# Performance work log

Measured on AMD Instinct MI355X. Metric: run time of the kernel, lower is better.

Reference implementation:

```python
import jax, jax.numpy as jnp
import numpy as np
import math

B, S, D, G, H_SEQ = 8, 4096, 1024, 64, 2048
TOP_K = 8


def setup_inputs() -> dict:
    key = jax.random.key(0)
    ks = jax.random.split(key, 10)
    K_curr = jax.random.normal(ks[0], (B, S, D), dtype=jnp.float32)
    V_curr = jax.random.normal(ks[1], (B, S, D), dtype=jnp.float32)
    K_prev = jax.random.normal(ks[2], (B, S, D), dtype=jnp.float32)
    V_prev = jax.random.normal(ks[3], (B, S, D), dtype=jnp.float32)
    h = jax.random.normal(ks[4], (B, H_SEQ, D), dtype=jnp.float32)
    momentum = jax.random.uniform(ks[5], (B, 1), dtype=jnp.float32)
    # unique active indices per batch (torch.scatter with dup idx is undefined)
    idx_keys = jax.random.split(ks[6], B)
    active_idx = jax.vmap(lambda k: jax.random.permutation(k, S)[:G])(idx_keys).astype(jnp.int32)
    # gate projection params: Linear(2, G), bias init = log(top_k - 1)
    Wk = jax.random.normal(ks[7], (G, 2), dtype=jnp.float32) * (1.0 / math.sqrt(2.0))
    Wv = jax.random.normal(ks[8], (G, 2), dtype=jnp.float32) * (1.0 / math.sqrt(2.0))
    bias_val = math.log(max(TOP_K - 1, 1))
    bk = jnp.full((G,), bias_val, dtype=jnp.float32)
    bv = jnp.full((G,), bias_val, dtype=jnp.float32)
    eta_init = 1.0 - 1.0 / H_SEQ
    logit_eta = jnp.asarray(math.log(eta_init / (1.0 - eta_init)), dtype=jnp.float32)
    alpha_logit = jnp.zeros((1,), dtype=jnp.float32)
    return {
        "K_curr": K_curr, "V_curr": V_curr, "K_prev": K_prev, "V_prev": V_prev,
        "h": h, "momentum": momentum, "active_idx": active_idx,
        "Wk": Wk, "bk": bk, "Wv": Wv, "bv": bv,
        "logit_eta": logit_eta, "alpha_logit": alpha_logit,
    }


def reference(K_curr, V_curr, K_prev, V_prev, h, momentum, active_idx,
              Wk, bk, Wv, bv, logit_eta, alpha_logit):
    scale = D ** (-0.5)
    idx = active_idx[..., None]  # [B, G, 1]
    # gather active slots: [B, G, D]
    K_active = jnp.take_along_axis(K_curr, idx, axis=1)
    K_prev_a = jnp.take_along_axis(K_prev, idx, axis=1)
    V_active = jnp.take_along_axis(V_curr, idx, axis=1)
    V_prev_a = jnp.take_along_axis(V_prev, idx, axis=1)

    q_probe = jnp.mean(h, axis=1)  # [B, D]

    def probe_surprise(X):
        # single-query attention probe over G slots
        attn = jax.nn.softmax(jnp.einsum('bd,bgd->bg', q_probe, X) * scale, axis=-1)
        pred = jnp.einsum('bg,bgd->bd', attn, X)
        return jnp.mean((pred - q_probe) ** 2, axis=-1, keepdims=True)  # [B, 1]

    k_surprise = probe_surprise(K_active)
    v_surprise = probe_surprise(V_active)

    alpha = jax.nn.sigmoid(alpha_logit)  # [1]
    combined = alpha * k_surprise + (1.0 - alpha) * v_surprise
    eta = jax.nn.sigmoid(logit_eta)
    new_momentum = eta * momentum + (1.0 - eta) * combined  # [B, 1]

    k_in = jnp.concatenate([k_surprise, new_momentum], axis=-1)  # [B, 2]
    v_in = jnp.concatenate([v_surprise, new_momentum], axis=-1)
    k_gate = jax.nn.sigmoid(k_in @ Wk.T + bk)[..., None]  # [B, G, 1]
    v_gate = jax.nn.sigmoid(v_in @ Wv.T + bv)[..., None]

    K_gated_a = k_gate * K_active + (1.0 - k_gate) * K_prev_a
    V_gated_a = v_gate * V_active + (1.0 - v_gate) * V_prev_a

    b_idx = jnp.arange(B)[:, None]  # [B, 1]
    K_gated = K_curr.at[b_idx, active_idx].set(K_gated_a)
    V_gated = V_curr.at[b_idx, active_idx].set(V_gated_a)
    return K_gated, V_gated, new_momentum
```

## Files before the change

kernel.cpp:

```cpp
#include <hip/hip_runtime.h>

#define BB 8
#define SS 4096
#define DD 1024
#define D4 256
#define GG 64
#define HH 2048
#define NCH 64
#define SCALE 0.03125f
#define BSD (8L * 4096L * 1024L)

__device__ __forceinline__ float sigmoidf_(float x) {
    return 1.0f / (1.0f + expf(-x));
}

__global__ __launch_bounds__(256) void reduce_h(const float* __restrict__ h,
                                                float* __restrict__ partial) {
    int blk = blockIdx.x;
    int b  = blk >> 6;
    int ch = blk & 63;
    int t  = threadIdx.x;
    const float4* h4 = (const float4*)h;
    int sbase = ch * (HH / NCH);
    long base = ((long)b * HH + sbase) * D4 + t;
    float4 acc = make_float4(0.f, 0.f, 0.f, 0.f);
#pragma unroll 4
    for (int i = 0; i < HH / NCH; ++i) {
        float4 v = h4[base + (long)i * D4];
        acc.x += v.x; acc.y += v.y; acc.z += v.z; acc.w += v.w;
    }
    ((float4*)partial)[(long)blk * D4 + t] = acc;
}

__global__ __launch_bounds__(256) void probe_kernel(
        const float* __restrict__ K_curr, const float* __restrict__ V_curr,
        const float* __restrict__ momentum, const int* __restrict__ active_idx,
        const float* __restrict__ Wk, const float* __restrict__ bk,
        const float* __restrict__ Wv, const float* __restrict__ bv,
        const float* __restrict__ logit_eta, const float* __restrict__ alpha_logit,
        const float* __restrict__ partial,
        float* __restrict__ gate_k, float* __restrict__ gate_v,
        float* __restrict__ out_m) {
    int b = blockIdx.x;
    int t = threadIdx.x;
    int wave = t >> 6;
    int lane = t & 63;

    __shared__ float q[DD];
    __shared__ float lg[GG];
    __shared__ float attn[GG];
    __shared__ float red[4];
    __shared__ float s_sur[2];

    float4 acc = make_float4(0.f, 0.f, 0.f, 0.f);
    const float4* p4 = (const float4*)partial;
#pragma unroll 8
    for (int ch = 0; ch < NCH; ++ch) {
        float4 v = p4[(long)(b * NCH + ch) * D4 + t];
        acc.x += v.x; acc.y += v.y; acc.z += v.z; acc.w += v.w;
    }
    const float invH = 1.0f / (float)HH;
    acc.x *= invH; acc.y *= invH; acc.z *= invH; acc.w *= invH;
    ((float4*)q)[t] = acc;
    __syncthreads();

    for (int which = 0; which < 2; ++which) {
        const float* X = which ? V_curr : K_curr;

        for (int gi = 0; gi < 16; ++gi) {
            int g = wave * 16 + gi;
            int idx = active_idx[b * GG + g];
            const float* row = X + ((long)b * SS + idx) * DD;
            float s = 0.f;
#pragma unroll
            for (int j = 0; j < 16; ++j) {
                int d = lane + 64 * j;
                s += q[d] * row[d];
            }
#pragma unroll
            for (int off = 32; off >= 1; off >>= 1) s += __shfl_xor(s, off);
            if (lane == 0) lg[g] = s * SCALE;
        }
        __syncthreads();

        if (t < 64) {
            float x = lg[t];
            float m = x;
#pragma unroll
            for (int off = 32; off >= 1; off >>= 1) m = fmaxf(m, __shfl_xor(m, off));
            float e = expf(x - m);
            float ssum = e;
#pragma unroll
            for (int off = 32; off >= 1; off >>= 1) ssum += __shfl_xor(ssum, off);
            attn[t] = e / ssum;
        }
        __syncthreads();

        const float4* X4 = (const float4*)(X + (long)b * SS * DD);
        float4 pred = make_float4(0.f, 0.f, 0.f, 0.f);
        for (int g = 0; g < GG; ++g) {
            int idx = active_idx[b * GG + g];
            float a = attn[g];
            float4 xv = X4[(long)idx * D4 + t];
            pred.x += a * xv.x; pred.y += a * xv.y;
            pred.z += a * xv.z; pred.w += a * xv.w;
        }
        float4 qv = ((const float4*)q)[t];
        float dx = pred.x - qv.x, dy = pred.y - qv.y;
        float dz = pred.z - qv.z, dw = pred.w - qv.w;
        float ss = dx * dx + dy * dy + dz * dz + dw * dw;
#pragma unroll
        for (int off = 32; off >= 1; off >>= 1) ss += __shfl_xor(ss, off);
        if (lane == 0) red[wave] = ss;
        __syncthreads();
        if (t == 0) s_sur[which] = (red[0] + red[1] + red[2] + red[3]) / (float)DD;
        __syncthreads();
    }

    float ks = s_sur[0], vs = s_sur[1];
    float alpha = sigmoidf_(alpha_logit[0]);
    float eta   = sigmoidf_(logit_eta[0]);
    float combined = alpha * ks + (1.0f - alpha) * vs;
    float new_m = eta * momentum[b] + (1.0f - eta) * combined;
    if (t == 0) out_m[b] = new_m;
    if (t < GG) {
        gate_k[b * GG + t] = sigmoidf_(Wk[t * 2 + 0] * ks + Wk[t * 2 + 1] * new_m + bk[t]);
        gate_v[b * GG + t] = sigmoidf_(Wv[t * 2 + 0] * vs + Wv[t * 2 + 1] * new_m + bv[t]);
    }
}

__global__ __launch_bounds__(256) void scatter_copy(
        const float* __restrict__ K_curr, const float* __restrict__ V_curr,
        const float* __restrict__ K_prev, const float* __restrict__ V_prev,
        const int* __restrict__ active_idx,
        const float* __restrict__ gate_k, const float* __restrict__ gate_v,
        float* __restrict__ outK, float* __restrict__ outV) {
    int r = blockIdx.x;
    int b = r >> 12;
    int s = r & 4095;
    int t = threadIdx.x;

    __shared__ int aidx[GG];
    if (t < GG) aidx[t] = active_idx[b * GG + t];
    __syncthreads();

    int g = -1;
#pragma unroll
    for (int j = 0; j < GG; ++j)
        if (aidx[j] == s) g = j;

    long off = (long)r * D4 + t;
    float4 kc = ((const float4*)K_curr)[off];
    float4 vc = ((const float4*)V_curr)[off];

    if (g >= 0) {
        float gk = gate_k[b * GG + g];
        float gv = gate_v[b * GG + g];
        float4 kp = ((const float4*)K_prev)[off];
        float4 vp = ((const float4*)V_prev)[off];
        kc.x = gk * kc.x + (1.0f - gk) * kp.x;
        kc.y = gk * kc.y + (1.0f - gk) * kp.y;
        kc.z = gk * kc.z + (1.0f - gk) * kp.z;
        kc.w = gk * kc.w + (1.0f - gk) * kp.w;
        vc.x = gv * vc.x + (1.0f - gv) * vp.x;
        vc.y = gv * vc.y + (1.0f - gv) * vp.y;
        vc.z = gv * vc.z + (1.0f - gv) * vp.z;
        vc.w = gv * vc.w + (1.0f - gv) * vp.w;
    }
    ((float4*)outK)[off] = kc;
    ((float4*)outV)[off] = vc;
}

extern "C" void kernel_launch(void* const* d_in, const int* in_sizes, int n_in,
                              void* d_out, int out_size, void* d_ws, size_t ws_size,
                              hipStream_t stream) {
    const float* K_curr      = (const float*)d_in[0];
    const float* V_curr      = (const float*)d_in[1];
    const float* K_prev      = (const float*)d_in[2];
    const float* V_prev      = (const float*)d_in[3];
    const float* h           = (const float*)d_in[4];
    const float* momentum    = (const float*)d_in[5];
    const int*   active_idx  = (const int*)d_in[6];
    const float* Wk          = (const float*)d_in[7];
    const float* bk          = (const float*)d_in[8];
    const float* Wv          = (const float*)d_in[9];
    const float* bv          = (const float*)d_in[10];
    const float* logit_eta   = (const float*)d_in[11];
    const float* alpha_logit = (const float*)d_in[12];

    float* out = (float*)d_out;
    float* ws  = (float*)d_ws;

    float* partial = ws;
    float* gate_k  = ws + (long)BB * NCH * DD;
    float* gate_v  = gate_k + BB * GG;

    reduce_h<<<BB * NCH, 256, 0, stream>>>(h, partial);

    probe_kernel<<<BB, 256, 0, stream>>>(K_curr, V_curr, momentum, active_idx,
                                         Wk, bk, Wv, bv, logit_eta, alpha_logit,
                                         partial, gate_k, gate_v,
                                         out + 2 * BSD);

    scatter_copy<<<BB * SS, 256, 0, stream>>>(K_curr, V_curr, K_prev, V_prev,
                                              active_idx, gate_k, gate_v,
                                              out, out + BSD);
}
```

Measured before the change: 635.9 us.

## Fuse reduce, probe and copy into one cooperative persistent kernel

After: 843.9 us. +32.7%, slower.

```diff
diff --git a/kernel.cpp b/kernel.cpp
--- a/kernel.cpp
+++ b/kernel.cpp
@@ -1,4 +1,7 @@
 #include <hip/hip_runtime.h>
+#include <hip/hip_cooperative_groups.h>
+
+namespace cg = cooperative_groups;
 
 #define BB 8
 #define SS 4096
@@ -6,33 +9,192 @@
 #define D4 256
 #define GG 64
 #define HH 2048
-#define NCH 64
 #define SCALE 0.03125f
 #define BSD (8L * 4096L * 1024L)
 
+#define NBLK 1024
+#define NCH 128
+#define ROWS_PER_CH (HH / NCH)
+#define NPROBE 16
+#define NCOPY (NBLK - NPROBE)
+#define TOTROWS (BB * SS)
+
+#define NCHL 64
+
 __device__ __forceinline__ float sigmoidf_(float x) {
     return 1.0f / (1.0f + expf(-x));
 }
 
-__global__ __launch_bounds__(256) void reduce_h(const float* __restrict__ h,
-                                                float* __restrict__ partial) {
+__global__ __launch_bounds__(256, 4) void fused_kernel(
+        const float* __restrict__ K_curr, const float* __restrict__ V_curr,
+        const float* __restrict__ K_prev, const float* __restrict__ V_prev,
+        const float* __restrict__ h, const float* __restrict__ momentum,
+        const int* __restrict__ active_idx,
+        const float* __restrict__ Wk, const float* __restrict__ bk,
+        const float* __restrict__ Wv, const float* __restrict__ bv,
+        const float* __restrict__ logit_eta, const float* __restrict__ alpha_logit,
+        float* __restrict__ partial, float* __restrict__ sur,
+        float* __restrict__ outK, float* __restrict__ outV,
+        float* __restrict__ outM) {
+    cg::grid_group grid = cg::this_grid();
+    int bid = blockIdx.x;
+    int t = threadIdx.x;
+
+    {
+        int b  = bid >> 7;
+        int ch = bid & (NCH - 1);
+        const float4* h4 = (const float4*)h;
+        long base = ((long)b * HH + (long)ch * ROWS_PER_CH) * D4 + t;
+        float4 acc = make_float4(0.f, 0.f, 0.f, 0.f);
+#pragma unroll
+        for (int i = 0; i < ROWS_PER_CH; ++i) {
+            float4 v = h4[base + (long)i * D4];
+            acc.x += v.x; acc.y += v.y; acc.z += v.z; acc.w += v.w;
+        }
+        ((float4*)partial)[(long)bid * D4 + t] = acc;
+    }
+    grid.sync();
+
+    if (bid < NPROBE) {
+        __shared__ float q[DD];
+        __shared__ float lg[GG];
+        __shared__ float attn[GG];
+        __shared__ float red[4];
+        __shared__ int aidx[GG];
+
+        int b = bid >> 1;
+        int which = bid & 1;
+        const float* X = which ? V_curr : K_curr;
+        int wave = t >> 6;
+        int lane = t & 63;
+
+        if (t < GG) aidx[t] = active_idx[b * GG + t];
+
+        float4 acc = make_float4(0.f, 0.f, 0.f, 0.f);
+        const float4* p4 = (const float4*)partial;
+#pragma unroll 8
+        for (int ch = 0; ch < NCH; ++ch) {
+            float4 v = p4[(long)(b * NCH + ch) * D4 + t];
+            acc.x += v.x; acc.y += v.y; acc.z += v.z; acc.w += v.w;
+        }
+        const float invH = 1.0f / (float)HH;
+        acc.x *= invH; acc.y *= invH; acc.z *= invH; acc.w *= invH;
+        ((float4*)q)[t] = acc;
+        __syncthreads();
+
+        const float4* q4 = (const float4*)q;
+        for (int gi = 0; gi < 16; ++gi) {
+            int g = wave * 16 + gi;
+            int idx = aidx[g];
+            const float4* row4 = (const float4*)(X + ((long)b * SS + idx) * DD);
+            float s = 0.f;
+#pragma unroll
+            for (int j = 0; j < 4; ++j) {
+                float4 rv = row4[lane + 64 * j];
+                float4 qv = q4[lane + 64 * j];
+                s += rv.x * qv.x + rv.y * qv.y + rv.z * qv.z + rv.w * qv.w;
+            }
+#pragma unroll
+            for (int off = 32; off >= 1; off >>= 1) s += __shfl_xor(s, off);
+            if (lane == 0) lg[g] = s * SCALE;
+        }
+        __syncthreads();
+
+        if (t < 64) {
+            float x = lg[t];
+            float m = x;
+#pragma unroll
+            for (int off = 32; off >= 1; off >>= 1) m = fmaxf(m, __shfl_xor(m, off));
+            float e = expf(x - m);
+            float ssum = e;
+#pragma unroll
+            for (int off = 32; off >= 1; off >>= 1) ssum += __shfl_xor(ssum, off);
+            attn[t] = e / ssum;
+        }
+        __syncthreads();
+
+        const float4* X4 = (const float4*)(X + (long)b * SS * DD);
+        float4 pred = make_float4(0.f, 0.f, 0.f, 0.f);
+        for (int g = 0; g < GG; ++g) {
+            int idx = aidx[g];
+            float a = attn[g];
+            float4 xv = X4[(long)idx * D4 + t];
+            pred.x += a * xv.x; pred.y += a * xv.y;
+            pred.z += a * xv.z; pred.w += a * xv.w;
+        }
+        float4 qv = ((const float4*)q)[t];
+        float dx = pred.x - qv.x, dy = pred.y - qv.y;
+        float dz = pred.z - qv.z, dw = pred.w - qv.w;
+        float ss = dx * dx + dy * dy + dz * dz + dw * dw;
+#pragma unroll
+        for (int off = 32; off >= 1; off >>= 1) ss += __shfl_xor(ss, off);
+        if (lane == 0) red[wave] = ss;
+        __syncthreads();
+        if (t == 0) sur[bid] = (red[0] + red[1] + red[2] + red[3]) / (float)DD;
+    } else {
+        const float4* kc4 = (const float4*)K_curr;
+        const float4* vc4 = (const float4*)V_curr;
+        float4* ok4 = (float4*)outK;
+        float4* ov4 = (float4*)outV;
+        for (int r = bid - NPROBE; r < TOTROWS; r += NCOPY) {
+            long off = (long)r * D4 + t;
+            ok4[off] = kc4[off];
+            ov4[off] = vc4[off];
+        }
+    }
+    grid.sync();
+
+    if (bid < BB * GG) {
+        int b = bid >> 6;
+        int g = bid & 63;
+        float ks = sur[2 * b + 0];
+        float vs = sur[2 * b + 1];
+        float alpha = sigmoidf_(alpha_logit[0]);
+        float eta   = sigmoidf_(logit_eta[0]);
+        float combined = alpha * ks + (1.0f - alpha) * vs;
+        float new_m = eta * momentum[b] + (1.0f - eta) * combined;
+        if (g == 0 && t == 0) outM[b] = new_m;
+        float gk = sigmoidf_(Wk[g * 2 + 0] * ks + Wk[g * 2 + 1] * new_m + bk[g]);
+        float gv = sigmoidf_(Wv[g * 2 + 0] * vs + Wv[g * 2 + 1] * new_m + bv[g]);
+        int idx = active_idx[b * GG + g];
+        long off = ((long)b * SS + idx) * D4 + t;
+        float4 kc = ((const float4*)K_curr)[off];
+        float4 kp = ((const float4*)K_prev)[off];
+        float4 vc = ((const float4*)V_curr)[off];
+        float4 vp = ((const float4*)V_prev)[off];
+        float4 ko, vo;
+        ko.x = gk * kc.x + (1.0f - gk) * kp.x;
+        ko.y = gk * kc.y + (1.0f - gk) * kp.y;
+        ko.z = gk * kc.z + (1.0f - gk) * kp.z;
+        ko.w = gk * kc.w + (1.0f - gk) * kp.w;
+        vo.x = gv * vc.x + (1.0f - gv) * vp.x;
+        vo.y = gv * vc.y + (1.0f - gv) * vp.y;
+        vo.z = gv * vc.z + (1.0f - gv) * vp.z;
+        vo.w = gv * vc.w + (1.0f - gv) * vp.w;
+        ((float4*)outK)[off] = ko;
+        ((float4*)outV)[off] = vo;
+    }
+}
+
+__global__ __launch_bounds__(256) void reduce_h_legacy(const float* __restrict__ h,
+                                                       float* __restrict__ partial) {
     int blk = blockIdx.x;
     int b  = blk >> 6;
     int ch = blk & 63;
     int t  = threadIdx.x;
     const float4* h4 = (const float4*)h;
-    int sbase = ch * (HH / NCH);
+    int sbase = ch * (HH / NCHL);
     long base = ((long)b * HH + sbase) * D4 + t;
     float4 acc = make_float4(0.f, 0.f, 0.f, 0.f);
 #pragma unroll 4
-    for (int i = 0; i < HH / NCH; ++i) {
+    for (int i = 0; i < HH / NCHL; ++i) {
         float4 v = h4[base + (long)i * D4];
         acc.x += v.x; acc.y += v.y; acc.z += v.z; acc.w += v.w;
     }
     ((float4*)partial)[(long)blk * D4 + t] = acc;
 }
 
-__global__ __launch_bounds__(256) void probe_kernel(
+__global__ __launch_bounds__(256) void probe_legacy(
         const float* __restrict__ K_curr, const float* __restrict__ V_curr,
         const float* __restrict__ momentum, const int* __restrict__ active_idx,
         const float* __restrict__ Wk, const float* __restrict__ bk,
@@ -55,8 +217,8 @@
     float4 acc = make_float4(0.f, 0.f, 0.f, 0.f);
     const float4* p4 = (const float4*)partial;
 #pragma unroll 8
-    for (int ch = 0; ch < NCH; ++ch) {
-        float4 v = p4[(long)(b * NCH + ch) * D4 + t];
+    for (int ch = 0; ch < NCHL; ++ch) {
+        float4 v = p4[(long)(b * NCHL + ch) * D4 + t];
         acc.x += v.x; acc.y += v.y; acc.z += v.z; acc.w += v.w;
     }
     const float invH = 1.0f / (float)HH;
@@ -66,7 +228,6 @@
 
     for (int which = 0; which < 2; ++which) {
         const float* X = which ? V_curr : K_curr;
-
         for (int gi = 0; gi < 16; ++gi) {
             int g = wave * 16 + gi;
             int idx = active_idx[b * GG + g];
@@ -129,7 +290,7 @@
     }
 }
 
-__global__ __launch_bounds__(256) void scatter_copy(
+__global__ __launch_bounds__(256) void scatter_legacy(
         const float* __restrict__ K_curr, const float* __restrict__ V_curr,
         const float* __restrict__ K_prev, const float* __restrict__ V_prev,
         const int* __restrict__ active_idx,
@@ -192,17 +353,34 @@
     float* ws  = (float*)d_ws;
 
     float* partial = ws;
-    float* gate_k  = ws + (long)BB * NCH * DD;
+    float* sur     = partial + (long)BB * NCH * DD;
+    float* gate_k  = sur + 16;
     float* gate_v  = gate_k + BB * GG;
-
-    reduce_h<<<BB * NCH, 256, 0, stream>>>(h, partial);
-
-    probe_kernel<<<BB, 256, 0, stream>>>(K_curr, V_curr, momentum, active_idx,
-                                         Wk, bk, Wv, bv, logit_eta, alpha_logit,
-                                         partial, gate_k, gate_v,
-                                         out + 2 * BSD);
-
-    scatter_copy<<<BB * SS, 256, 0, stream>>>(K_curr, V_curr, K_prev, V_prev,
-                                              active_idx, gate_k, gate_v,
-                                              out, out + BSD);
-}
+    float* oldpart = gate_v + BB * GG;
+
+    float* outK = out;
+    float* outV = out + BSD;
+    float* outM = out + 2 * BSD;
+
+    void* args[] = {
+        (void*)&K_curr, (void*)&V_curr, (void*)&K_prev, (void*)&V_prev,
+        (void*)&h, (void*)&momentum, (void*)&active_idx,
+        (void*)&Wk, (void*)&bk, (void*)&Wv, (void*)&bv,
+        (void*)&logit_eta, (void*)&alpha_logit,
+        (void*)&partial, (void*)&sur,
+        (void*)&outK, (void*)&outV, (void*)&outM
+    };
+
+    hipError_t err = hipLaunchCooperativeKernel((const void*)fused_kernel,
+                                                dim3(NBLK), dim3(256),
+                                                args, 0, stream);
+    if (err != hipSuccess) {
+        reduce_h_legacy<<<BB * NCHL, 256, 0, stream>>>(h, oldpart);
+        probe_legacy<<<BB, 256, 0, stream>>>(K_curr, V_curr, momentum, active_idx,
+                                             Wk, bk, Wv, bv, logit_eta, alpha_logit,
+                                             oldpart, gate_k, gate_v, outM);
+        scatter_legacy<<<BB * SS, 256, 0, stream>>>(K_curr, V_curr, K_prev, V_prev,
+                                                    active_idx, gate_k, gate_v,
+                                                    outK, outV);
+    }
+}
```
